# Performance work log

Measured on AMD Instinct MI355X. Metric: run time of the kernel, lower is better.

Reference implementation:

```python
import jax, jax.numpy as jnp
import numpy as np

B, L, DIN, D = 16, 4096, 64, 64
HA, HL, WIN, NL, K, DFF = 8, 4, 64, 3, 3, 128


def _ln(x, g, b):
    m = x.mean(-1, keepdims=True)
    v = ((x - m) ** 2).mean(-1, keepdims=True)
    return (x - m) * jax.lax.rsqrt(v + 1e-5) * g + b


def _dynamic_conv(x, kernels, w1, b1, w2, b2):
    # x: (B, C, H, 1); kernels: (K, C_out, C_in, 3, 3)
    b, c, h, w = x.shape
    pooled = x.mean(axis=(2, 3))                      # AdaptiveAvgPool2d(1)
    hdn = jax.nn.relu(pooled @ w1.T + b1)             # 1x1 conv C -> C//4
    attn = jax.nn.softmax(hdn @ w2.T + b2, axis=-1)   # (B, K) kernel weights
    kw = kernels.reshape(K * c, c, 3, 3)              # run all K kernels in one conv
    out = jax.lax.conv_general_dilated(x, kw, (1, 1), [(1, 1), (1, 1)],
                                       dimension_numbers=('NCHW', 'OIHW', 'NCHW'))
    out = out.reshape(b, K, c, h, w)
    return jnp.einsum('bkchw,bk->bchw', out, attn)


def _agent_attn(x, wv, bv, an_bias, na_bias):
    # agent_num = 1: a single pooled agent token per sample
    b, n, c = x.shape
    hd = c // HA
    scale = hd ** -0.5
    v = x @ wv + bv
    lepe = v                                          # get_lepe uses the same linear
    qh = x.reshape(b, n, HA, hd).transpose(0, 2, 1, 3)  # (B, HA, L, hd)
    kh = qh
    vh = v.reshape(b, n, HA, hd).transpose(0, 2, 1, 3)
    agent = x.mean(axis=1).reshape(b, HA, 1, hd)      # AdaptiveAvgPool1d(1) over L
    a_attn = jax.nn.softmax(jnp.einsum('bhad,bhnd->bhan', agent * scale, kh) + an_bias, axis=-1)
    agent_v = jnp.einsum('bhan,bhnd->bhad', a_attn, vh)            # (B, HA, 1, hd)
    nb = jnp.swapaxes(na_bias, -1, -2)                              # (HA, L, 1)
    q_attn = jax.nn.softmax(jnp.einsum('bhnd,bhad->bhna', qh * scale, agent) + nb, axis=-1)
    out = jnp.einsum('bhna,bhad->bhnd', q_attn, agent_v)
    return out.transpose(0, 2, 1, 3).reshape(b, n, c) + lepe


def _local_attn(x, wq, bq, wk, bk, wv, bv, wo, bo):
    b, n, d = x.shape
    dk = d // HL
    nw = n // WIN

    def heads(w, bias):
        return (x @ w + bias).reshape(b, nw, WIN, HL, dk).transpose(0, 3, 1, 2, 4)

    q, k, v = heads(wq, bq), heads(wk, bk), heads(wv, bv)
    s = jnp.einsum('bhwid,bhwjd->bhwij', q, k) / (dk ** 0.5)        # per-window scores
    a = jax.nn.softmax(s, axis=-1)
    o = jnp.einsum('bhwij,bhwjd->bhwid', a, v)
    o = o.transpose(0, 2, 3, 1, 4).reshape(b, n, d)
    return o @ wo + bo


def setup_inputs() -> dict:
    key = jax.random.key(0)
    ks = iter(jax.random.split(key, 40))
    nrm = lambda shape, s=0.02: jax.random.normal(next(ks), shape, jnp.float32) * s
    Cr = DIN // 4
    return {
        'x': jax.random.normal(next(ks), (B, L, DIN), jnp.float32),
        'dc_kernels': nrm((3, K, DIN, DIN, 3, 3), 0.05),
        'dc_w1': nrm((3, Cr, DIN)), 'dc_b1': jnp.zeros((3, Cr), jnp.float32),
        'dc_w2': nrm((3, K, Cr)), 'dc_b2': jnp.zeros((3, K), jnp.float32),
        'emb_w': nrm((DIN, D)), 'emb_b': jnp.zeros((D,), jnp.float32),
        'getv_w': nrm((NL, D, D)), 'getv_b': jnp.zeros((NL, D), jnp.float32),
        'an_bias': nrm((NL, HA, 1, L)), 'na_bias': nrm((NL, HA, 1, L)),
        'wq': nrm((NL, D, D)), 'bq': jnp.zeros((NL, D), jnp.float32),
        'wk': nrm((NL, D, D)), 'bk': jnp.zeros((NL, D), jnp.float32),
        'wv': nrm((NL, D, D)), 'bv': jnp.zeros((NL, D), jnp.float32),
        'wo': nrm((NL, D, D)), 'bo': jnp.zeros((NL, D), jnp.float32),
        'ff_w1': nrm((NL, D, DFF)), 'ff_b1': jnp.zeros((NL, DFF), jnp.float32),
        'ff_w2': nrm((NL, DFF, D)), 'ff_b2': jnp.zeros((NL, D), jnp.float32),
        'ln1_g': jnp.ones((NL, D), jnp.float32), 'ln1_b': jnp.zeros((NL, D), jnp.float32),
        'ln2_g': jnp.ones((NL, D), jnp.float32), 'ln2_b': jnp.zeros((NL, D), jnp.float32),
    }


def reference(x, dc_kernels, dc_w1, dc_b1, dc_w2, dc_b2, emb_w, emb_b,
              getv_w, getv_b, an_bias, na_bias,
              wq, bq, wk, bk, wv, bv, wo, bo,
              ff_w1, ff_b1, ff_w2, ff_b2, ln1_g, ln1_b, ln2_g, ln2_b):
    # dynamic multi-kernel convs on (B, C=d_input, H=L, W=1)
    h = x.transpose(0, 2, 1)[..., None]
    for i in range(3):
        h = _dynamic_conv(h, dc_kernels[i], dc_w1[i], dc_b1[i], dc_w2[i], dc_b2[i])
    h = h[..., 0].transpose(0, 2, 1)
    # data embedding (value_linear=True, value_sqrt=False, pos_emb=False)
    h = h @ emb_w + emb_b
    for i in range(NL):
        attn = _agent_attn(h, getv_w[i], getv_b[i], an_bias[i], na_bias[i]) + \
               _local_attn(h, wq[i], bq[i], wk[i], bk[i], wv[i], bv[i], wo[i], bo[i])
        h1 = _ln(h + attn, ln1_g[i], ln1_b[i])
        ffo = jax.nn.relu(h1 @ ff_w1[i] + ff_b1[i]) @ ff_w2[i] + ff_b2[i]
        h = _ln(h1 + ffo, ln2_g[i], ln2_b[i])
    return h
```

## Files before the change

### kernel.cpp

```cpp
#include <hip/hip_runtime.h>

#define BB 16
#define LL 4096
#define DD 64

typedef const float* __restrict__ cfp;
typedef float* __restrict__ fp;
typedef const ushort* __restrict__ cup;
typedef ushort* __restrict__ up;

typedef __attribute__((ext_vector_type(8))) short bf16x8;
typedef __attribute__((ext_vector_type(4))) float f32x4;
#define MFMA16(a, b, c) __builtin_amdgcn_mfma_f32_16x16x32_bf16(a, b, c, 0, 0, 0)

__device__ __forceinline__ f32x4 zf4(){ f32x4 z; z[0]=0.f; z[1]=0.f; z[2]=0.f; z[3]=0.f; return z; }

union frag_u { bf16x8 v; uint2 u2[2]; uint u[4]; };

__device__ __forceinline__ float4 ld4(const float* p){ return *reinterpret_cast<const float4*>(p); }

__device__ __forceinline__ ushort f2bf(float f){
  uint u = __float_as_uint(f);
  return (ushort)((u + 0x7FFFu + ((u >> 16) & 1u)) >> 16);
}
__device__ __forceinline__ float bf2f(ushort u){
  return __uint_as_float(((uint)u) << 16);
}
__device__ __forceinline__ uint packf2(float a, float b){
  return (uint)f2bf(a) | ((uint)f2bf(b) << 16);
}
__device__ __forceinline__ uint2 pack4(float4 v){
  return make_uint2(packf2(v.x, v.y), packf2(v.z, v.w));
}
__device__ __forceinline__ bf16x8 ldfrag(const ushort* p){ return *reinterpret_cast<const bf16x8*>(p); }

__global__ __launch_bounds__(256) void k_pack(cfp wq, cfp wk, cfp wv, cfp getv, cfp wo,
                                              cfp fw1, cfp fw2, cfp embw,
                                              up dst, up dstE) {
  int layer = blockIdx.y;
  int e = blockIdx.x*256 + threadIdx.x;
  if (e >= 36864) {
    int rem = e - 36864;
    int j = rem & 7, lane = (rem >> 3) & 63, rest = rem >> 9;
    int nt = rest & 3, ks = rest >> 2;
    int k = ks*32 + ((lane >> 4) << 3) + j, n = nt*16 + (lane & 15);
    dstE[rem] = f2bf(embw[k*64 + n]);
    return;
  }
  const float* W; int N, rem;
  if (e < 20480) {
    int mm = e >> 12; rem = e & 4095;
    W = (mm==0?wq: mm==1?wk: mm==2?wv: mm==3?getv: wo) + layer*4096; N = 64;
  } else if (e < 28672) {
    rem = e - 20480; W = fw1 + layer*8192; N = 128;
  } else {
    rem = e - 28672; W = fw2 + layer*8192; N = 64;
  }
  int NT = N >> 4;
  int j = rem & 7, lane = (rem >> 3) & 63, rest = rem >> 9;
  int nt = rest % NT, ks = rest / NT;
  int k = ks*32 + ((lane >> 4) << 3) + j, n = nt*16 + (lane & 15);
  dst[(size_t)layer*36864 + e] = f2bf(W[(size_t)k*N + n]);
}

__global__ __launch_bounds__(256) void k_pool_part(cfp h, fp pp) {
  int b = blockIdx.x, gblk = blockIdx.y, t = threadIdx.x;
  int c = t & 63, r = t >> 6;
  const float* base = h + ((size_t)b*LL + (size_t)gblk*256)*64;
  float acc = 0.f;
  for (int l = r; l < 256; l += 4) acc += base[(size_t)l*64 + c];
  __shared__ float red[4][64];
  red[r][c] = acc; __syncthreads();
  if (t < 64) pp[(b*16 + gblk)*64 + t] = red[0][t]+red[1][t]+red[2][t]+red[3][t];
}

__global__ __launch_bounds__(256) void k_weff(cfp pp, int chunks,
                                              cfp w1, cfp b1, cfp w2, cfp b2,
                                              cfp kern, up weffB) {
  int b = blockIdx.x, t = threadIdx.x;
  __shared__ float pooled[64], hdn[16], attn[3];
  if (t < 64) {
    float s = 0.f;
    for (int g = 0; g < chunks; ++g) s += pp[((size_t)b*chunks + g)*64 + t];
    pooled[t] = s * (1.f/4096.f);
  }
  __syncthreads();
  if (t < 16) {
    float a = b1[t];
    for (int c = 0; c < 64; ++c) a += pooled[c]*w1[t*64 + c];
    hdn[t] = fmaxf(a, 0.f);
  }
  __syncthreads();
  if (t < 3) {
    float a = b2[t];
    for (int j = 0; j < 16; ++j) a += hdn[j]*w2[t*16 + j];
    attn[t] = a;
  }
  __syncthreads();
  if (t == 0) {
    float m = fmaxf(attn[0], fmaxf(attn[1], attn[2]));
    float e0 = __expf(attn[0]-m), e1 = __expf(attn[1]-m), e2 = __expf(attn[2]-m);
    float s = e0+e1+e2;
    attn[0]=e0/s; attn[1]=e1/s; attn[2]=e2/s;
  }
  __syncthreads();
  float a0=attn[0], a1=attn[1], a2=attn[2];
  int e0i = blockIdx.y * 1536;
  for (int e = e0i + t; e < e0i + 1536; e += 256) {
    int j = e & 7, lane = (e >> 3) & 63, nt = (e >> 9) & 3, ks = e >> 11;
    int k = ks*32 + ((lane >> 4) << 3) + j;
    int co = nt*16 + (lane & 15);
    int kh = k >> 6, ci = k & 63;
    size_t base = ((size_t)co*64 + ci)*9 + kh*3 + 1;
    float v = a0*kern[base] + a1*kern[base + 36864] + a2*kern[base + 2*36864];
    weffB[(size_t)b*12288 + e] = f2bf(v);
  }
}

__device__ __forceinline__ void conv_mfma(const ushort* Ts, const ushort* wb,
                                          int band, int lr, int lg, int l, f32x4 acc[4]) {
  #pragma unroll
  for (int nt = 0; nt < 4; ++nt) acc[nt] = zf4();
  #pragma unroll
  for (int ks = 0; ks < 6; ++ks) {
    int k8 = ks*32 + lg*8;
    int kh = k8 >> 6, ci = k8 & 63;
    bf16x8 a = ldfrag(Ts + (band + lr + kh)*72 + ci);
    #pragma unroll
    for (int nt = 0; nt < 4; ++nt)
      acc[nt] = MFMA16(a, ldfrag(wb + ((ks*4+nt)*64 + l)*8), acc[nt]);
  }
}

__global__ __launch_bounds__(256) void k_conv0(cfp hin, cup weffB, up houtB, fp pp) {
  int b = blockIdx.x, wblk = blockIdx.y, t = threadIdx.x;
  int n0 = wblk*64;
  __shared__ ushort Ts[66*72];
  __shared__ float red[64*17];
  for (int idx = t; idx < 1056; idx += 256) {
    int r = idx >> 4, c4 = (idx & 15)*4, gr = n0 - 1 + r;
    float4 v = make_float4(0.f,0.f,0.f,0.f);
    if (gr >= 0 && gr < LL) v = ld4(hin + ((size_t)b*LL + gr)*64 + c4);
    *(uint2*)(Ts + r*72 + c4) = pack4(v);
  }
  __syncthreads();
  int w = t >> 6, l = t & 63, band = w*16, lr = l & 15, lg = l >> 4;
  f32x4 acc[4];
  conv_mfma(Ts, weffB + (size_t)b*12288, band, lr, lg, l, acc);
  __syncthreads();
  #pragma unroll
  for (int nt = 0; nt < 4; ++nt) {
    int co = nt*16 + lr;
    float part = 0.f;
    #pragma unroll
    for (int reg = 0; reg < 4; ++reg) {
      int row = band + lg*4 + reg;
      Ts[row*72 + co] = f2bf(acc[nt][reg]);
      part += acc[nt][reg];
    }
    red[co*17 + w*4 + lg] = part;
  }
  __syncthreads();
  for (int idx = t; idx < 512; idx += 256) {
    int r = idx >> 3, c8 = (idx & 7)*8;
    *(uint4*)(houtB + ((size_t)b*LL + n0 + r)*64 + c8) = *(const uint4*)(Ts + r*72 + c8);
  }
  if (t < 64) {
    float s = 0.f;
    #pragma unroll
    for (int g = 0; g < 16; ++g) s += red[t*17 + g];
    pp[((size_t)b*64 + wblk)*64 + t] = s;
  }
}

__global__ __launch_bounds__(256) void k_conv1(cup hinB, cup weffB, up houtB, fp pp) {
  int b = blockIdx.x, wblk = blockIdx.y, t = threadIdx.x;
  int n0 = wblk*64;
  __shared__ ushort Ts[66*72];
  __shared__ float red[64*17];
  for (int idx = t; idx < 528; idx += 256) {
    int r = idx >> 3, c8 = (idx & 7)*8, gr = n0 - 1 + r;
    uint4 v = make_uint4(0u,0u,0u,0u);
    if (gr >= 0 && gr < LL) v = *(const uint4*)(hinB + ((size_t)b*LL + gr)*64 + c8);
    *(uint4*)(Ts + r*72 + c8) = v;
  }
  __syncthreads();
  int w = t >> 6, l = t & 63, band = w*16, lr = l & 15, lg = l >> 4;
  f32x4 acc[4];
  conv_mfma(Ts, weffB + (size_t)b*12288, band, lr, lg, l, acc);
  __syncthreads();
  #pragma unroll
  for (int nt = 0; nt < 4; ++nt) {
    int co = nt*16 + lr;
    float part = 0.f;
    #pragma unroll
    for (int reg = 0; reg < 4; ++reg) {
      int row = band + lg*4 + reg;
      Ts[row*72 + co] = f2bf(acc[nt][reg]);
      part += acc[nt][reg];
    }
    red[co*17 + w*4 + lg] = part;
  }
  __syncthreads();
  for (int idx = t; idx < 512; idx += 256) {
    int r = idx >> 3, c8 = (idx & 7)*8;
    *(uint4*)(houtB + ((size_t)b*LL + n0 + r)*64 + c8) = *(const uint4*)(Ts + r*72 + c8);
  }
  if (t < 64) {
    float s = 0.f;
    #pragma unroll
    for (int g = 0; g < 16; ++g) s += red[t*17 + g];
    pp[((size_t)b*64 + wblk)*64 + t] = s;
  }
}

__global__ __launch_bounds__(256) void k_conv2e(cup hinB, cup weffB, cup wE, cfp embb,
                                                up houtB, fp pp) {
  int b = blockIdx.x, wblk = blockIdx.y, t = threadIdx.x;
  int n0 = wblk*64;
  __shared__ ushort Ts[66*72];
  __shared__ float red[64*17];
  for (int idx = t; idx < 528; idx += 256) {
    int r = idx >> 3, c8 = (idx & 7)*8, gr = n0 - 1 + r;
    uint4 v = make_uint4(0u,0u,0u,0u);
    if (gr >= 0 && gr < LL) v = *(const uint4*)(hinB + ((size_t)b*LL + gr)*64 + c8);
    *(uint4*)(Ts + r*72 + c8) = v;
  }
  __syncthreads();
  int w = t >> 6, l = t & 63, band = w*16, lr = l & 15, lg = l >> 4;
  f32x4 acc[4];
  conv_mfma(Ts, weffB + (size_t)b*12288, band, lr, lg, l, acc);
  __syncthreads();
  #pragma unroll
  for (int nt = 0; nt < 4; ++nt) {
    int co = nt*16 + lr;
    #pragma unroll
    for (int reg = 0; reg < 4; ++reg)
      Ts[(band + lg*4 + reg)*72 + co] = f2bf(acc[nt][reg]);
  }
  __syncthreads();
  f32x4 ea[4];
  #pragma unroll
  for (int nt = 0; nt < 4; ++nt) ea[nt] = zf4();
  #pragma unroll
  for (int ks = 0; ks < 2; ++ks) {
    bf16x8 a = ldfrag(Ts + (band + lr)*72 + ks*32 + lg*8);
    #pragma unroll
    for (int nt = 0; nt < 4; ++nt)
      ea[nt] = MFMA16(a, ldfrag(wE + ((ks*4+nt)*64 + l)*8), ea[nt]);
  }
  #pragma unroll
  for (int nt = 0; nt < 4; ++nt) {
    int col = nt*16 + lr;
    float bc = embb[col], part = 0.f;
    #pragma unroll
    for (int reg = 0; reg < 4; ++reg) {
      int row = band + lg*4 + reg;
      float y = ea[nt][reg] + bc;
      Ts[row*72 + col] = f2bf(y);
      part += y;
    }
    red[col*17 + w*4 + lg] = part;
  }
  __syncthreads();
  for (int idx = t; idx < 512; idx += 256) {
    int r = idx >> 3, c8 = (idx & 7)*8;
    *(uint4*)(houtB + ((size_t)b*LL + n0 + r)*64 + c8) = *(const uint4*)(Ts + r*72 + c8);
  }
  if (t < 64) {
    float s = 0.f;
    #pragma unroll
    for (int g = 0; g < 16; ++g) s += red[t*17 + g];
    pp[((size_t)b*64 + wblk)*64 + t] = s;
  }
}

__global__ __launch_bounds__(256) void k_agent2(cup h16, cfp anb, cfp pp,
                                                fp pm, fp pe, fp pw) {
  int b = blockIdx.x, ch = blockIdx.y, t = threadIdx.x;
  int w = t >> 6, l = t & 63;
  __shared__ float means_s[64];
  __shared__ float sc[8][258];
  __shared__ float red4[4][64];
  __shared__ float esp[8][33];
  __shared__ float mcs[8], ess[8];
  __shared__ float wred[4][8][64];
  {
    float acc = 0.f;
    for (int c = w; c < 64; c += 4) acc += pp[((size_t)b*64 + c)*64 + l];
    red4[w][l] = acc;
  }
  __syncthreads();
  if (t < 64) means_s[t] = (red4[0][t]+red4[1][t]+red4[2][t]+red4[3][t])
                           * (1.f/4096.f) * 0.35355339059327373f;
  __syncthreads();
  const ushort* hb = h16 + ((size_t)b*LL + (size_t)ch*256)*64;
  int g8 = l >> 3, k8 = l & 7;
  float ms8[8];
  #pragma unroll
  for (int j = 0; j < 8; ++j) ms8[j] = means_s[k8*8 + j];
  #pragma unroll
  for (int it = 0; it < 8; ++it) {
    int n = w*64 + it*8 + g8;
    uint4 hv = *(const uint4*)(hb + (size_t)n*64 + k8*8);
    float d = bf2f((ushort)(hv.x & 0xffffu))*ms8[0] + bf2f((ushort)(hv.x >> 16))*ms8[1]
            + bf2f((ushort)(hv.y & 0xffffu))*ms8[2] + bf2f((ushort)(hv.y >> 16))*ms8[3]
            + bf2f((ushort)(hv.z & 0xffffu))*ms8[4] + bf2f((ushort)(hv.z >> 16))*ms8[5]
            + bf2f((ushort)(hv.w & 0xffffu))*ms8[6] + bf2f((ushort)(hv.w >> 16))*ms8[7];
    sc[k8][n] = d;
  }
  __syncthreads();
  int hh = t >> 5, j0 = (t & 31) * 8;
  const float* ab = anb + (size_t)hh*LL + ch*256 + j0;
  float loc[8];
  float mx = -1e30f;
  #pragma unroll
  for (int k = 0; k < 8; ++k) {
    loc[k] = sc[hh][j0 + k] + ab[k];
    mx = fmaxf(mx, loc[k]);
  }
  esp[hh][t & 31] = mx;
  __syncthreads();
  if (t < 8) {
    float m = -1e30f;
    for (int k = 0; k < 32; ++k) m = fmaxf(m, esp[t][k]);
    mcs[t] = m;
  }
  __syncthreads();
  {
    float M = mcs[hh], s = 0.f;
    #pragma unroll
    for (int k = 0; k < 8; ++k) {
      float e = __expf(loc[k] - M);
      sc[hh][j0 + k] = e;
      s += e;
    }
    esp[hh][t & 31] = s;
  }
  __syncthreads();
  if (t < 8) {
    float s = 0.f;
    for (int k = 0; k < 32; ++k) s += esp[t][k];
    ess[t] = s;
  }
  float acc8[8] = {};
  for (int i = 0; i < 64; ++i) {
    int n = w*64 + i;
    float x = bf2f(hb[(size_t)n*64 + l]);
    #pragma unroll
    for (int q = 0; q < 8; ++q) acc8[q] = fmaf(sc[q][n], x, acc8[q]);
  }
  __syncthreads();
  #pragma unroll
  for (int q = 0; q < 8; ++q) wred[w][q][l] = acc8[q];
  __syncthreads();
  for (int o = t; o < 512; o += 256) {
    int q = o >> 6, ll = o & 63;
    pw[(((size_t)b*16 + ch)*8 + q)*64 + ll] =
        wred[0][q][ll]+wred[1][q][ll]+wred[2][q][ll]+wred[3][q][ll];
  }
  if (t < 8) {
    pe[((size_t)b*16 + ch)*8 + t] = ess[t];
    pm[((size_t)b*16 + ch)*8 + t] = mcs[t];
  }
}

template<bool OUT_BF16>
__global__ __launch_bounds__(256, 4) void k_layer(
    cup h16, cfp pm, cfp pe, cfp pw, cfp getv, cfp getvb, cup wB,
    cfp bq, cfp bk, cfp bv, cfp bo,
    cfp g1, cfp be1, cfp b1, cfp b2, cfp g2, cfp be2,
    fp Y, up Y16, fp pp) {
  __shared__ float smem[10048];
  ushort* HsB  = (ushort*)(smem);
  ushort* Qp   = (ushort*)(smem + 2304);
  ushort* Kp   = (ushort*)(smem + 4864);
  ushort* Vt   = (ushort*)(smem + 7424);
  float*  sums = smem + 9728;
  float*  agvs = smem + 9984;
  float*  wm   = smem + 7424;
  float*  msden= smem + 7944;
  ushort* OB   = (ushort*)(smem + 7424);
  float*  red  = smem + 7424;
  ushort* HidB = (ushort*)(smem + 2304);

  int t = threadIdx.x;
  size_t n0 = (size_t)blockIdx.x*64;
  int b = (int)(n0 >> 12);
  int w = t >> 6, l = t & 63, band = w*16, lr = l & 15, lg = l >> 4;

  #pragma unroll
  for (int it = 0; it < 2; ++it) {
    int idx = it*256 + t, r = idx >> 3, c8 = (idx & 7)*8;
    *(uint4*)(HsB + r*72 + c8) = *(const uint4*)(h16 + (n0 + r)*64 + c8);
  }
  if (t < 8) {
    float M = -1e30f;
    for (int c = 0; c < 16; ++c) M = fmaxf(M, pm[((size_t)b*16+c)*8 + t]);
    float d = 0.f;
    for (int c = 0; c < 16; ++c)
      d += pe[((size_t)b*16+c)*8 + t] * __expf(pm[((size_t)b*16+c)*8 + t] - M);
    msden[t] = M; msden[8+t] = d;
  }
  __syncthreads();
  for (int o = t; o < 512; o += 256) {
    int q = o >> 6, l2 = o & 63;
    float M = msden[q], s = 0.f;
    for (int c = 0; c < 16; ++c)
      s += pw[(((size_t)b*16+c)*8 + q)*64 + l2] * __expf(pm[((size_t)b*16+c)*8 + q] - M);
    wm[q*65 + l2] = s / msden[8+q];
  }
  __syncthreads();
  if (t < 64) {
    int q = t >> 3;
    float a = getvb[t];
    for (int c = 0; c < 64; ++c) a = fmaf(wm[q*65 + c], getv[c*64 + t], a);
    agvs[t] = a;
  }
  __syncthreads();

  f32x4 ka[4], va[4], qa[4], la[4];
  #pragma unroll
  for (int nt = 0; nt < 4; ++nt) {
    ka[nt] = zf4(); va[nt] = zf4(); qa[nt] = zf4(); la[nt] = zf4();
  }
  #pragma unroll
  for (int ks = 0; ks < 2; ++ks) {
    bf16x8 a = ldfrag(HsB + (band + lr)*72 + ks*32 + lg*8);
    #pragma unroll
    for (int nt = 0; nt < 4; ++nt) {
      int fo = ((ks*4 + nt)*64 + l)*8;
      qa[nt] = MFMA16(a, ldfrag(wB + fo),         qa[nt]);
      ka[nt] = MFMA16(a, ldfrag(wB + 4096 + fo),  ka[nt]);
      va[nt] = MFMA16(a, ldfrag(wB + 8192 + fo),  va[nt]);
      la[nt] = MFMA16(a, ldfrag(wB + 12288 + fo), la[nt]);
    }
  }
  #pragma unroll
  for (int nt = 0; nt < 4; ++nt) {
    int col = nt*16 + lr;
    float bkc = bk[col], bvc = bv[col], bqc = bq[col];
    #pragma unroll
    for (int reg = 0; reg < 4; ++reg) {
      int tok = band + 4*lg + reg;
      Kp[nt*1280 + tok*20 + lr] = f2bf(ka[nt][reg] + bkc);
      Qp[nt*1280 + tok*20 + lr] = f2bf((qa[nt][reg] + bqc) * 0.25f);
    }
    int tok0 = band + 4*lg;
    *(uint2*)(Vt + nt*1152 + lr*72 + tok0) =
        make_uint2(packf2(va[nt][0]+bvc, va[nt][1]+bvc),
                   packf2(va[nt][2]+bvc, va[nt][3]+bvc));
  }
  __syncthreads();

  {
    frag_u kaf[4], qbf[4], vbf[4], pf;
    #pragma unroll
    for (int tt = 0; tt < 4; ++tt) {
      kaf[tt].u2[0] = *(const uint2*)(Kp + w*1280 + (tt*16+lr)*20 + lg*4);
      kaf[tt].u[2] = 0; kaf[tt].u[3] = 0;
      qbf[tt].u2[0] = *(const uint2*)(Qp + w*1280 + (tt*16+lr)*20 + lg*4);
      qbf[tt].u[2] = 0; qbf[tt].u[3] = 0;
      vbf[tt].u2[0] = *(const uint2*)(Vt + w*1152 + lr*72 + tt*16 + lg*4);
      vbf[tt].u[2] = 0; vbf[tt].u[3] = 0;
    }
    f32x4 st[4][4];
    #pragma unroll
    for (int kt = 0; kt < 4; ++kt)
      #pragma unroll
      for (int qt = 0; qt < 4; ++qt) {
        f32x4 z = zf4();
        st[kt][qt] = MFMA16(kaf[kt].v, qbf[qt].v, z);
      }
    f32x4 oacc[4];
    #pragma unroll
    for (int qt = 0; qt < 4; ++qt) {
      float M = -1e30f;
      #pragma unroll
      for (int kt = 0; kt < 4; ++kt)
        #pragma unroll
        for (int reg = 0; reg < 4; ++reg) M = fmaxf(M, st[kt][qt][reg]);
      M = fmaxf(M, __shfl_xor(M, 16));
      M = fmaxf(M, __shfl_xor(M, 32));
      float s = 0.f;
      #pragma unroll
      for (int kt = 0; kt < 4; ++kt)
        #pragma unroll
        for (int reg = 0; reg < 4; ++reg) {
          float e = __expf(st[kt][qt][reg] - M);
          st[kt][qt][reg] = e; s += e;
        }
      s += __shfl_xor(s, 16);
      s += __shfl_xor(s, 32);
      if (lg == 0) sums[w*64 + qt*16 + lr] = s;
      oacc[qt] = zf4();
    }
    #pragma unroll
    for (int qt = 0; qt < 4; ++qt)
      #pragma unroll
      for (int kt = 0; kt < 4; ++kt) {
        pf.u[0] = packf2(st[kt][qt][0], st[kt][qt][1]);
        pf.u[1] = packf2(st[kt][qt][2], st[kt][qt][3]);
        pf.u[2] = 0; pf.u[3] = 0;
        oacc[qt] = MFMA16(pf.v, vbf[kt].v, oacc[qt]);
      }
    __syncthreads();
    #pragma unroll
    for (int qt = 0; qt < 4; ++qt)
      #pragma unroll
      for (int reg = 0; reg < 4; ++reg) {
        int q = qt*16 + 4*lg + reg;
        OB[q*72 + band + lr] = f2bf(oacc[qt][reg] / sums[w*64 + q]);
      }
  }
  __syncthreads();

  float comb[4][4];
  {
    f32x4 wa[4];
    #pragma unroll
    for (int nt = 0; nt < 4; ++nt) wa[nt] = zf4();
    #pragma unroll
    for (int ks = 0; ks < 2; ++ks) {
      bf16x8 a = ldfrag(OB + (band + lr)*72 + ks*32 + lg*8);
      #pragma unroll
      for (int nt = 0; nt < 4; ++nt)
        wa[nt] = MFMA16(a, ldfrag(wB + 16384 + ((ks*4+nt)*64 + l)*8), wa[nt]);
    }
    #pragma unroll
    for (int nt = 0; nt < 4; ++nt) {
      int col = nt*16 + lr;
      float cadd = bo[col] + agvs[col] + getvb[col];
      #pragma unroll
      for (int reg = 0; reg < 4; ++reg) {
        int row = band + lg*4 + reg;
        comb[nt][reg] = wa[nt][reg] + la[nt][reg] + cadd + bf2f(HsB[row*72 + col]);
      }
    }
  }
  {
    float mean1[4], rstd1[4];
    #pragma unroll
    for (int reg = 0; reg < 4; ++reg) {
      float s = comb[0][reg]+comb[1][reg]+comb[2][reg]+comb[3][reg];
      float qq = comb[0][reg]*comb[0][reg]+comb[1][reg]*comb[1][reg]
               + comb[2][reg]*comb[2][reg]+comb[3][reg]*comb[3][reg];
      s += __shfl_xor(s,1); qq += __shfl_xor(qq,1);
      s += __shfl_xor(s,2); qq += __shfl_xor(qq,2);
      s += __shfl_xor(s,4); qq += __shfl_xor(qq,4);
      s += __shfl_xor(s,8); qq += __shfl_xor(qq,8);
      float mn = s*0.015625f;
      mean1[reg] = mn;
      rstd1[reg] = rsqrtf(qq*0.015625f - mn*mn + 1e-5f);
    }
    #pragma unroll
    for (int nt = 0; nt < 4; ++nt) {
      int col = nt*16 + lr;
      float gg = g1[col], bb = be1[col];
      #pragma unroll
      for (int reg = 0; reg < 4; ++reg) {
        int row = band + lg*4 + reg;
        float h1 = (comb[nt][reg]-mean1[reg])*rstd1[reg]*gg + bb;
        HsB[row*72 + col] = f2bf(h1);
      }
    }
  }
  __syncthreads();

  {
    f32x4 fa[8];
    #pragma unroll
    for (int nt = 0; nt < 8; ++nt) fa[nt] = zf4();
    #pragma unroll
    for (int ks = 0; ks < 2; ++ks) {
      bf16x8 a = ldfrag(HsB + (band + lr)*72 + ks*32 + lg*8);
      #pragma unroll
      for (int nt = 0; nt < 8; ++nt)
        fa[nt] = MFMA16(a, ldfrag(wB + 20480 + ((ks*8+nt)*64 + l)*8), fa[nt]);
    }
    #pragma unroll
    for (int nt = 0; nt < 8; ++nt) {
      int col = nt*16 + lr;
      float b1c = b1[col];
      #pragma unroll
      for (int reg = 0; reg < 4; ++reg) {
        int row = band + lg*4 + reg;
        HidB[row*136 + col] = f2bf(fmaxf(fa[nt][reg] + b1c, 0.f));
      }
    }
  }
  __syncthreads();

  {
    f32x4 f2[4];
    #pragma unroll
    for (int nt = 0; nt < 4; ++nt) f2[nt] = zf4();
    #pragma unroll
    for (int ks = 0; ks < 4; ++ks) {
      bf16x8 a = ldfrag(HidB + (band + lr)*136 + ks*32 + lg*8);
      #pragma unroll
      for (int nt = 0; nt < 4; ++nt)
        f2[nt] = MFMA16(a, ldfrag(wB + 28672 + ((ks*4+nt)*64 + l)*8), f2[nt]);
    }
    float c2[4][4];
    #pragma unroll
    for (int nt = 0; nt < 4; ++nt) {
      int col = nt*16 + lr;
      float b2c = b2[col];
      #pragma unroll
      for (int reg = 0; reg < 4; ++reg) {
        int row = band + lg*4 + reg;
        c2[nt][reg] = f2[nt][reg] + b2c + bf2f(HsB[row*72 + col]);
      }
    }
    float mean2[4], rstd2[4];
    #pragma unroll
    for (int reg = 0; reg < 4; ++reg) {
      float s = c2[0][reg]+c2[1][reg]+c2[2][reg]+c2[3][reg];
      float qq = c2[0][reg]*c2[0][reg]+c2[1][reg]*c2[1][reg]
               + c2[2][reg]*c2[2][reg]+c2[3][reg]*c2[3][reg];
      s += __shfl_xor(s,1); qq += __shfl_xor(qq,1);
      s += __shfl_xor(s,2); qq += __shfl_xor(qq,2);
      s += __shfl_xor(s,4); qq += __shfl_xor(qq,4);
      s += __shfl_xor(s,8); qq += __shfl_xor(qq,8);
      float mn = s*0.015625f;
      mean2[reg] = mn;
      rstd2[reg] = rsqrtf(qq*0.015625f - mn*mn + 1e-5f);
    }
    __syncthreads();
    #pragma unroll
    for (int nt = 0; nt < 4; ++nt) {
      int col = nt*16 + lr;
      float gg = g2[col], bb = be2[col];
      float part = 0.f;
      #pragma unroll
      for (int reg = 0; reg < 4; ++reg) {
        int row = band + lg*4 + reg;
        float y = (c2[nt][reg]-mean2[reg])*rstd2[reg]*gg + bb;
        if (OUT_BF16) Y16[(n0 + row)*64 + col] = f2bf(y);
        else          Y[(n0 + row)*64 + col] = y;
        part += y;
      }
      red[col*17 + w*4 + lg] = part;
    }
  }
  __syncthreads();
  if (t < 64) {
    float s = 0.f;
    #pragma unroll
    for (int g = 0; g < 16; ++g) s += red[t*17 + g];
    pp[(size_t)blockIdx.x*64 + t] = s;
  }
}

extern "C" void kernel_launch(void* const* d_in, const int* in_sizes, int n_in,
                              void* d_out, int out_size, void* d_ws, size_t ws_size,
                              hipStream_t stream) {
  (void)in_sizes; (void)n_in; (void)out_size; (void)ws_size;
  const float* x    = (const float*)d_in[0];
  const float* dck  = (const float*)d_in[1];
  const float* dcw1 = (const float*)d_in[2];
  const float* dcb1 = (const float*)d_in[3];
  const float* dcw2 = (const float*)d_in[4];
  const float* dcb2 = (const float*)d_in[5];
  const float* embw = (const float*)d_in[6];
  const float* embb = (const float*)d_in[7];
  const float* getvw= (const float*)d_in[8];
  const float* getvb= (const float*)d_in[9];
  const float* anb  = (const float*)d_in[10];
  const float* wq = (const float*)d_in[12]; const float* bq = (const float*)d_in[13];
  const float* wk = (const float*)d_in[14]; const float* bk = (const float*)d_in[15];
  const float* wv = (const float*)d_in[16]; const float* bv = (const float*)d_in[17];
  const float* wo = (const float*)d_in[18]; const float* bo = (const float*)d_in[19];
  const float* fw1= (const float*)d_in[20]; const float* fb1= (const float*)d_in[21];
  const float* fw2= (const float*)d_in[22]; const float* fb2= (const float*)d_in[23];
  const float* g1 = (const float*)d_in[24]; const float* be1= (const float*)d_in[25];
  const float* g2 = (const float*)d_in[26]; const float* be2= (const float*)d_in[27];

  float* out = (float*)d_out;
  float* ws  = (float*)d_ws;
  float* pp   = ws;
  float* pm   = pp + 65536;
  float* pe   = pm + 2048;
  float* pw   = pe + 2048;
  ushort* hB0  = (ushort*)(pw + 131072);
  ushort* hB1  = hB0 + (size_t)BB*LL*64;
  ushort* weffB= hB1 + (size_t)BB*LL*64;
  ushort* wsB  = weffB + (size_t)BB*12288;
  ushort* wsE  = wsB + (size_t)3*36864;

  dim3 blk(256);
  const int NT = BB*LL/64;

  k_pack<<<dim3(160, 3), blk, 0, stream>>>(wq, wk, wv, getvw, wo, fw1, fw2, embw, wsB, wsE);

  k_pool_part<<<dim3(BB,16), blk, 0, stream>>>(x, pp);
  k_weff<<<dim3(BB,8), blk, 0, stream>>>(pp, 16, dcw1, dcb1, dcw2, dcb2, dck, weffB);
  k_conv0<<<dim3(BB,64), blk, 0, stream>>>(x, weffB, hB0, pp);
  k_weff<<<dim3(BB,8), blk, 0, stream>>>(pp, 64, dcw1 + 1024, dcb1 + 16, dcw2 + 48, dcb2 + 3,
                                         dck + 110592, weffB);
  k_conv1<<<dim3(BB,64), blk, 0, stream>>>(hB0, weffB, hB1, pp);
  k_weff<<<dim3(BB,8), blk, 0, stream>>>(pp, 64, dcw1 + 2048, dcb1 + 32, dcw2 + 96, dcb2 + 6,
                                         dck + 221184, weffB);
  k_conv2e<<<dim3(BB,64), blk, 0, stream>>>(hB1, weffB, wsE, embb, hB0, pp);

  ushort* h  = hB0;
  ushort* hn = hB1;
  for (int i = 0; i < 3; ++i) {
    k_agent2<<<dim3(BB,16), blk, 0, stream>>>(h, anb + (size_t)i*8*4096, pp, pm, pe, pw);
    if (i == 2) {
      k_layer<false><<<NT, blk, 0, stream>>>(h, pm, pe, pw, getvw + i*4096, getvb + i*64,
                                             wsB + (size_t)i*36864,
                                             bq + i*64, bk + i*64, bv + i*64, bo + i*64,
                                             g1 + i*64, be1 + i*64, fb1 + i*128, fb2 + i*64,
                                             g2 + i*64, be2 + i*64, out, nullptr, pp);
    } else {
      k_layer<true><<<NT, blk, 0, stream>>>(h, pm, pe, pw, getvw + i*4096, getvb + i*64,
                                            wsB + (size_t)i*36864,
                                            bq + i*64, bk + i*64, bv + i*64, bo + i*64,
                                            g1 + i*64, be1 + i*64, fb1 + i*128, fb2 + i*64,
                                            g2 + i*64, be2 + i*64, nullptr, hn, pp);
    }
    ushort* tmp = h; h = hn; hn = tmp;
  }
}
```

Baseline: 202.2 us.

## Fuse three dynamic convs via analytic pooled-sum attention precompute

Pooled means after conv 0 and conv 1 are now derived analytically from the input column sums and boundary rows, since conv is linear. That lets all three softmax attention weight sets be computed up front in one small kernel. The three convs plus the embedding are then fused into one kernel that recomputes halo rows (4 on each side) in shared memory, removing two intermediate bf16 HBM round trips and four launches. The cost is extra halo compute and larger shared memory per block, plus a serial per-batch attention kernel.

```diff
diff --git a/kernel.cpp b/kernel.cpp
--- a/kernel.cpp
+++ b/kernel.cpp
@@ -74,17 +74,9 @@
   if (t < 64) pp[(b*16 + gblk)*64 + t] = red[0][t]+red[1][t]+red[2][t]+red[3][t];
 }
 
-__global__ __launch_bounds__(256) void k_weff(cfp pp, int chunks,
-                                              cfp w1, cfp b1, cfp w2, cfp b2,
-                                              cfp kern, up weffB) {
-  int b = blockIdx.x, t = threadIdx.x;
-  __shared__ float pooled[64], hdn[16], attn[3];
-  if (t < 64) {
-    float s = 0.f;
-    for (int g = 0; g < chunks; ++g) s += pp[((size_t)b*chunks + g)*64 + t];
-    pooled[t] = s * (1.f/4096.f);
-  }
-  __syncthreads();
+__device__ __forceinline__ void tiny_mlp3(int t, const float* __restrict__ pooled,
+                                          cfp w1, cfp b1, cfp w2, cfp b2,
+                                          float* attn, float* hdn) {
   if (t < 16) {
     float a = b1[t];
     for (int c = 0; c < 64; ++c) a += pooled[c]*w1[t*64 + c];
@@ -104,8 +96,90 @@
     attn[0]=e0/s; attn[1]=e1/s; attn[2]=e2/s;
   }
   __syncthreads();
-  float a0=attn[0], a1=attn[1], a2=attn[2];
-  int e0i = blockIdx.y * 1536;
+}
+
+__global__ __launch_bounds__(256) void k_attns(cfp pp, cfp x, cfp dcw1, cfp dcb1,
+                                               cfp dcw2, cfp dcb2, cfp dck, fp attns) {
+  int b = blockIdx.x, t = threadIdx.x;
+  __shared__ float S[64], e0v[64], e1v[64], em0[64], em1[64];
+  __shared__ float h10[64], h1m[64], Sn[64];
+  __shared__ float pooled[64], hdn[16], attn[3], redu[256];
+  const float* xb = x + (size_t)b*LL*64;
+  if (t < 64) {
+    float s = 0.f;
+    for (int g = 0; g < 16; ++g) s += pp[((size_t)b*16 + g)*64 + t];
+    S[t] = s;
+    pooled[t] = s * (1.f/4096.f);
+    e0v[t] = xb[t];
+    e1v[t] = xb[64 + t];
+    em0[t] = xb[(size_t)(LL-2)*64 + t];
+    em1[t] = xb[(size_t)(LL-1)*64 + t];
+  }
+  __syncthreads();
+  tiny_mlp3(t, pooled, dcw1, dcb1, dcw2, dcb2, attn, hdn);
+  if (t < 3) attns[b*9 + t] = attn[t];
+  {
+    int co = t & 63, q = t >> 6;
+    float a0 = attn[0], a1 = attn[1], a2 = attn[2];
+    float ph0=0.f, phm=0.f, pS=0.f;
+    cfp kb = dck;
+    for (int ci = q*16; ci < q*16 + 16; ++ci) {
+      size_t base = ((size_t)co*64 + ci)*9 + 1;
+      float k00=kb[base],       k01=kb[base+3],       k02=kb[base+6];
+      float k10=kb[base+36864], k11=kb[base+36867],   k12=kb[base+36870];
+      float k20=kb[base+73728], k21=kb[base+73731],   k22=kb[base+73734];
+      float w0 = a0*k00 + a1*k10 + a2*k20;
+      float w1 = a0*k01 + a1*k11 + a2*k21;
+      float w2 = a0*k02 + a1*k12 + a2*k22;
+      ph0 += w1*e0v[ci] + w2*e1v[ci];
+      phm += w0*em0[ci] + w1*em1[ci];
+      pS  += w0*(S[ci]-em1[ci]) + w1*S[ci] + w2*(S[ci]-e0v[ci]);
+    }
+    redu[t] = ph0; __syncthreads();
+    if (t < 64) h10[t] = redu[t]+redu[64+t]+redu[128+t]+redu[192+t];
+    __syncthreads();
+    redu[t] = phm; __syncthreads();
+    if (t < 64) h1m[t] = redu[t]+redu[64+t]+redu[128+t]+redu[192+t];
+    __syncthreads();
+    redu[t] = pS; __syncthreads();
+    if (t < 64) {
+      Sn[t] = redu[t]+redu[64+t]+redu[128+t]+redu[192+t];
+      pooled[t] = Sn[t] * (1.f/4096.f);
+    }
+    __syncthreads();
+  }
+  tiny_mlp3(t, pooled, dcw1+1024, dcb1+16, dcw2+48, dcb2+3, attn, hdn);
+  if (t < 3) attns[b*9 + 3 + t] = attn[t];
+  {
+    int co = t & 63, q = t >> 6;
+    float a0 = attn[0], a1 = attn[1], a2 = attn[2];
+    float pS = 0.f;
+    cfp kb = dck + 110592;
+    for (int ci = q*16; ci < q*16 + 16; ++ci) {
+      size_t base = ((size_t)co*64 + ci)*9 + 1;
+      float k00=kb[base],       k01=kb[base+3],       k02=kb[base+6];
+      float k10=kb[base+36864], k11=kb[base+36867],   k12=kb[base+36870];
+      float k20=kb[base+73728], k21=kb[base+73731],   k22=kb[base+73734];
+      float w0 = a0*k00 + a1*k10 + a2*k20;
+      float w1 = a0*k01 + a1*k11 + a2*k21;
+      float w2 = a0*k02 + a1*k12 + a2*k22;
+      pS += w0*(Sn[ci]-h1m[ci]) + w1*Sn[ci] + w2*(Sn[ci]-h10[ci]);
+    }
+    redu[t] = pS; __syncthreads();
+    if (t < 64) pooled[t] = (redu[t]+redu[64+t]+redu[128+t]+redu[192+t]) * (1.f/4096.f);
+    __syncthreads();
+  }
+  tiny_mlp3(t, pooled, dcw1+2048, dcb1+32, dcw2+96, dcb2+6, attn, hdn);
+  if (t < 3) attns[b*9 + 6 + t] = attn[t];
+}
+
+__global__ __launch_bounds__(256) void k_wefff(cfp attns, cfp dck, up weffB) {
+  int b = blockIdx.x, stage = blockIdx.y >> 3, slice = blockIdx.y & 7, t = threadIdx.x;
+  float a0 = attns[b*9 + stage*3 + 0];
+  float a1 = attns[b*9 + stage*3 + 1];
+  float a2 = attns[b*9 + stage*3 + 2];
+  cfp kern = dck + (size_t)stage*110592;
+  int e0i = slice*1536;
   for (int e = e0i + t; e < e0i + 1536; e += 256) {
     int j = e & 7, lane = (e >> 3) & 63, nt = (e >> 9) & 3, ks = e >> 11;
     int k = ks*32 + ((lane >> 4) << 3) + j;
@@ -113,7 +187,7 @@
     int kh = k >> 6, ci = k & 63;
     size_t base = ((size_t)co*64 + ci)*9 + kh*3 + 1;
     float v = a0*kern[base] + a1*kern[base + 36864] + a2*kern[base + 2*36864];
-    weffB[(size_t)b*12288 + e] = f2bf(v);
+    weffB[((size_t)stage*16 + b)*12288 + e] = f2bf(v);
   }
 }
 
@@ -132,140 +206,106 @@
   }
 }
 
-__global__ __launch_bounds__(256) void k_conv0(cfp hin, cup weffB, up houtB, fp pp) {
+__global__ __launch_bounds__(256) void k_convF(cfp x, cup weffB, cup wE, cfp embb,
+                                               up houtB, fp pp) {
   int b = blockIdx.x, wblk = blockIdx.y, t = threadIdx.x;
   int n0 = wblk*64;
-  __shared__ ushort Ts[66*72];
+  __shared__ ushort TsA[84*72];
+  __shared__ ushort TsB[84*72];
   __shared__ float red[64*17];
-  for (int idx = t; idx < 1056; idx += 256) {
-    int r = idx >> 4, c4 = (idx & 15)*4, gr = n0 - 1 + r;
+  int w = t >> 6, l = t & 63, lr = l & 15, lg = l >> 4;
+
+  for (int idx = t; idx < 1344; idx += 256) {
+    int r = idx >> 4, c4 = (idx & 15)*4;
+    int g = n0 - 4 + r;
     float4 v = make_float4(0.f,0.f,0.f,0.f);
-    if (gr >= 0 && gr < LL) v = ld4(hin + ((size_t)b*LL + gr)*64 + c4);
-    *(uint2*)(Ts + r*72 + c4) = pack4(v);
-  }
-  __syncthreads();
-  int w = t >> 6, l = t & 63, band = w*16, lr = l & 15, lg = l >> 4;
-  f32x4 acc[4];
-  conv_mfma(Ts, weffB + (size_t)b*12288, band, lr, lg, l, acc);
-  __syncthreads();
-  #pragma unroll
-  for (int nt = 0; nt < 4; ++nt) {
-    int co = nt*16 + lr;
-    float part = 0.f;
-    #pragma unroll
-    for (int reg = 0; reg < 4; ++reg) {
-      int row = band + lg*4 + reg;
-      Ts[row*72 + co] = f2bf(acc[nt][reg]);
-      part += acc[nt][reg];
-    }
-    red[co*17 + w*4 + lg] = part;
+    if (r >= 1 && r <= 70 && g >= 0 && g < LL) v = ld4(x + ((size_t)b*LL + g)*64 + c4);
+    *(uint2*)(TsA + r*72 + c4) = pack4(v);
+  }
+  for (int idx = t; idx < 32; idx += 256) {
+    int r = 82 + (idx >> 4), c4 = (idx & 15)*4;
+    *(uint2*)(TsB + r*72 + c4) = make_uint2(0u,0u);
+  }
+  __syncthreads();
+
+  {
+    const ushort* wb = weffB + (size_t)b*12288;
+    for (int bi = w; bi < 5; bi += 4) {
+      int band = 2 + bi*16;
+      f32x4 acc[4];
+      conv_mfma(TsA, wb, band - 1, lr, lg, l, acc);
+      #pragma unroll
+      for (int nt = 0; nt < 4; ++nt)
+        #pragma unroll
+        for (int reg = 0; reg < 4; ++reg) {
+          int row = band + lg*4 + reg;
+          int g = n0 - 4 + row;
+          float v = (g >= 0 && g < LL) ? acc[nt][reg] : 0.f;
+          TsB[row*72 + nt*16 + lr] = f2bf(v);
+        }
+    }
+  }
+  __syncthreads();
+  {
+    const ushort* wb = weffB + (size_t)(16 + b)*12288;
+    for (int bi = w; bi < 5; bi += 4) {
+      int band = 3 + bi*16;
+      f32x4 acc[4];
+      conv_mfma(TsB, wb, band - 1, lr, lg, l, acc);
+      #pragma unroll
+      for (int nt = 0; nt < 4; ++nt)
+        #pragma unroll
+        for (int reg = 0; reg < 4; ++reg) {
+          int row = band + lg*4 + reg;
+          int g = n0 - 4 + row;
+          float v = (g >= 0 && g < LL) ? acc[nt][reg] : 0.f;
+          TsA[row*72 + nt*16 + lr] = f2bf(v);
+        }
+    }
+  }
+  __syncthreads();
+  {
+    const ushort* wb = weffB + (size_t)(32 + b)*12288;
+    int band = 4 + w*16;
+    f32x4 acc[4];
+    conv_mfma(TsA, wb, band - 1, lr, lg, l, acc);
+    #pragma unroll
+    for (int nt = 0; nt < 4; ++nt)
+      #pragma unroll
+      for (int reg = 0; reg < 4; ++reg)
+        TsB[(band + lg*4 + reg)*72 + nt*16 + lr] = f2bf(acc[nt][reg]);
+  }
+  __syncthreads();
+  {
+    int band = 4 + w*16;
+    f32x4 ea[4];
+    #pragma unroll
+    for (int nt = 0; nt < 4; ++nt) ea[nt] = zf4();
+    #pragma unroll
+    for (int ks = 0; ks < 2; ++ks) {
+      bf16x8 a = ldfrag(TsB + (band + lr)*72 + ks*32 + lg*8);
+      #pragma unroll
+      for (int nt = 0; nt < 4; ++nt)
+        ea[nt] = MFMA16(a, ldfrag(wE + ((ks*4+nt)*64 + l)*8), ea[nt]);
+    }
+    #pragma unroll
+    for (int nt = 0; nt < 4; ++nt) {
+      int col = nt*16 + lr;
+      float bc = embb[col], part = 0.f;
+      #pragma unroll
+      for (int reg = 0; reg < 4; ++reg) {
+        int row = band + lg*4 + reg;
+        float y = ea[nt][reg] + bc;
+        TsA[row*72 + col] = f2bf(y);
+        part += y;
+      }
+      red[col*17 + w*4 + lg] = part;
+    }
   }
   __syncthreads();
   for (int idx = t; idx < 512; idx += 256) {
     int r = idx >> 3, c8 = (idx & 7)*8;
-    *(uint4*)(houtB + ((size_t)b*LL + n0 + r)*64 + c8) = *(const uint4*)(Ts + r*72 + c8);
-  }
-  if (t < 64) {
-    float s = 0.f;
-    #pragma unroll
-    for (int g = 0; g < 16; ++g) s += red[t*17 + g];
-    pp[((size_t)b*64 + wblk)*64 + t] = s;
-  }
-}
-
-__global__ __launch_bounds__(256) void k_conv1(cup hinB, cup weffB, up houtB, fp pp) {
-  int b = blockIdx.x, wblk = blockIdx.y, t = threadIdx.x;
-  int n0 = wblk*64;
-  __shared__ ushort Ts[66*72];
-  __shared__ float red[64*17];
-  for (int idx = t; idx < 528; idx += 256) {
-    int r = idx >> 3, c8 = (idx & 7)*8, gr = n0 - 1 + r;
-    uint4 v = make_uint4(0u,0u,0u,0u);
-    if (gr >= 0 && gr < LL) v = *(const uint4*)(hinB + ((size_t)b*LL + gr)*64 + c8);
-    *(uint4*)(Ts + r*72 + c8) = v;
-  }
-  __syncthreads();
-  int w = t >> 6, l = t & 63, band = w*16, lr = l & 15, lg = l >> 4;
-  f32x4 acc[4];
-  conv_mfma(Ts, weffB + (size_t)b*12288, band, lr, lg, l, acc);
-  __syncthreads();
-  #pragma unroll
-  for (int nt = 0; nt < 4; ++nt) {
-    int co = nt*16 + lr;
-    float part = 0.f;
-    #pragma unroll
-    for (int reg = 0; reg < 4; ++reg) {
-      int row = band + lg*4 + reg;
-      Ts[row*72 + co] = f2bf(acc[nt][reg]);
-      part += acc[nt][reg];
-    }
-    red[co*17 + w*4 + lg] = part;
-  }
-  __syncthreads();
-  for (int idx = t; idx < 512; idx += 256) {
-    int r = idx >> 3, c8 = (idx & 7)*8;
-    *(uint4*)(houtB + ((size_t)b*LL + n0 + r)*64 + c8) = *(const uint4*)(Ts + r*72 + c8);
-  }
-  if (t < 64) {
-    float s = 0.f;
-    #pragma unroll
-    for (int g = 0; g < 16; ++g) s += red[t*17 + g];
-    pp[((size_t)b*64 + wblk)*64 + t] = s;
-  }
-}
-
-__global__ __launch_bounds__(256) void k_conv2e(cup hinB, cup weffB, cup wE, cfp embb,
-                                                up houtB, fp pp) {
-  int b = blockIdx.x, wblk = blockIdx.y, t = threadIdx.x;
-  int n0 = wblk*64;
-  __shared__ ushort Ts[66*72];
-  __shared__ float red[64*17];
-  for (int idx = t; idx < 528; idx += 256) {
-    int r = idx >> 3, c8 = (idx & 7)*8, gr = n0 - 1 + r;
-    uint4 v = make_uint4(0u,0u,0u,0u);
-    if (gr >= 0 && gr < LL) v = *(const uint4*)(hinB + ((size_t)b*LL + gr)*64 + c8);
-    *(uint4*)(Ts + r*72 + c8) = v;
-  }
-  __syncthreads();
-  int w = t >> 6, l = t & 63, band = w*16, lr = l & 15, lg = l >> 4;
-  f32x4 acc[4];
-  conv_mfma(Ts, weffB + (size_t)b*12288, band, lr, lg, l, acc);
-  __syncthreads();
-  #pragma unroll
-  for (int nt = 0; nt < 4; ++nt) {
-    int co = nt*16 + lr;
-    #pragma unroll
-    for (int reg = 0; reg < 4; ++reg)
-      Ts[(band + lg*4 + reg)*72 + co] = f2bf(acc[nt][reg]);
-  }
-  __syncthreads();
-  f32x4 ea[4];
-  #pragma unroll
-  for (int nt = 0; nt < 4; ++nt) ea[nt] = zf4();
-  #pragma unroll
-  for (int ks = 0; ks < 2; ++ks) {
-    bf16x8 a = ldfrag(Ts + (band + lr)*72 + ks*32 + lg*8);
-    #pragma unroll
-    for (int nt = 0; nt < 4; ++nt)
-      ea[nt] = MFMA16(a, ldfrag(wE + ((ks*4+nt)*64 + l)*8), ea[nt]);
-  }
-  #pragma unroll
-  for (int nt = 0; nt < 4; ++nt) {
-    int col = nt*16 + lr;
-    float bc = embb[col], part = 0.f;
-    #pragma unroll
-    for (int reg = 0; reg < 4; ++reg) {
-      int row = band + lg*4 + reg;
-      float y = ea[nt][reg] + bc;
-      Ts[row*72 + col] = f2bf(y);
-      part += y;
-    }
-    red[col*17 + w*4 + lg] = part;
-  }
-  __syncthreads();
-  for (int idx = t; idx < 512; idx += 256) {
-    int r = idx >> 3, c8 = (idx & 7)*8;
-    *(uint4*)(houtB + ((size_t)b*LL + n0 + r)*64 + c8) = *(const uint4*)(Ts + r*72 + c8);
+    *(uint4*)(houtB + ((size_t)b*LL + n0 + r)*64 + c8) = *(const uint4*)(TsA + (r+4)*72 + c8);
   }
   if (t < 64) {
     float s = 0.f;
@@ -346,9 +386,9 @@
   float acc8[8] = {};
   for (int i = 0; i < 64; ++i) {
     int n = w*64 + i;
-    float x = bf2f(hb[(size_t)n*64 + l]);
-    #pragma unroll
-    for (int q = 0; q < 8; ++q) acc8[q] = fmaf(sc[q][n], x, acc8[q]);
+    float xv = bf2f(hb[(size_t)n*64 + l]);
+    #pragma unroll
+    for (int q = 0; q < 8; ++q) acc8[q] = fmaf(sc[q][n], xv, acc8[q]);
   }
   __syncthreads();
   #pragma unroll
@@ -679,30 +719,25 @@
 
   float* out = (float*)d_out;
   float* ws  = (float*)d_ws;
-  float* pp   = ws;
-  float* pm   = pp + 65536;
-  float* pe   = pm + 2048;
-  float* pw   = pe + 2048;
-  ushort* hB0  = (ushort*)(pw + 131072);
+  float* pp    = ws;
+  float* pm    = pp + 65536;
+  float* pe    = pm + 2048;
+  float* pw    = pe + 2048;
+  float* attns = pw + 131072;
+  ushort* hB0  = (ushort*)(attns + 256);
   ushort* hB1  = hB0 + (size_t)BB*LL*64;
   ushort* weffB= hB1 + (size_t)BB*LL*64;
-  ushort* wsB  = weffB + (size_t)BB*12288;
+  ushort* wsB  = weffB + (size_t)3*BB*12288;
   ushort* wsE  = wsB + (size_t)3*36864;
 
   dim3 blk(256);
   const int NT = BB*LL/64;
 
   k_pack<<<dim3(160, 3), blk, 0, stream>>>(wq, wk, wv, getvw, wo, fw1, fw2, embw, wsB, wsE);
-
   k_pool_part<<<dim3(BB,16), blk, 0, stream>>>(x, pp);
-  k_weff<<<dim3(BB,8), blk, 0, stream>>>(pp, 16, dcw1, dcb1, dcw2, dcb2, dck, weffB);
-  k_conv0<<<dim3(BB,64), blk, 0, stream>>>(x, weffB, hB0, pp);
-  k_weff<<<dim3(BB,8), blk, 0, stream>>>(pp, 64, dcw1 + 1024, dcb1 + 16, dcw2 + 48, dcb2 + 3,
-                                         dck + 110592, weffB);
-  k_conv1<<<dim3(BB,64), blk, 0, stream>>>(hB0, weffB, hB1, pp);
-  k_weff<<<dim3(BB,8), blk, 0, stream>>>(pp, 64, dcw1 + 2048, dcb1 + 32, dcw2 + 96, dcb2 + 6,
-                                         dck + 221184, weffB);
-  k_conv2e<<<dim3(BB,64), blk, 0, stream>>>(hB1, weffB, wsE, embb, hB0, pp);
+  k_attns<<<BB, blk, 0, stream>>>(pp, x, dcw1, dcb1, dcw2, dcb2, dck, attns);
+  k_wefff<<<dim3(BB,24), blk, 0, stream>>>(attns, dck, weffB);
+  k_convF<<<dim3(BB,64), blk, 0, stream>>>(x, weffB, wsE, embb, hB0, pp);
 
   ushort* h  = hB0;
   ushort* hn = hB1;
```

Measured after the change: 211.1 us. +4.4%, slower.
